# Kernel tuning notes

Hardware: AMD Instinct MI355X
Metric: run time of the kernel (lower is better)

Reference implementation:

```python
import jax, jax.numpy as jnp
from jax import lax
import numpy as np

NS, NC = 12, 4            # n_state, n_ctrl
NSC = NS + NC             # tau = [x; u]
T, B = 50, 2048
U_LO, U_HI = -1.0, 1.0
LQR_ITERS = 3             # qp_iter-style outer LQR iterations
N_LS = 5                  # max_linesearch_iter
LS_DECAY = 0.5            # linesearch_decay


def setup_inputs() -> dict:
    key = jax.random.key(0)
    k0, k1, k2, k3, k4 = jax.random.split(key, 5)
    x0 = jax.random.normal(k0, (B, NS), jnp.float32)
    # PD quadratic cost: C = 0.1 * A A^T + I  (symmetric positive definite)
    A = jax.random.normal(k1, (T, B, NSC, NSC), jnp.float32) * (1.0 / np.sqrt(NSC))
    C = 0.1 * jnp.einsum('tbik,tbjk->tbij', A, A) + jnp.eye(NSC, dtype=jnp.float32)
    c = jax.random.normal(k2, (T, B, NSC), jnp.float32)
    # Near-identity stable linear dynamics x' = F [x;u] + f
    F = 0.02 * jax.random.normal(k3, (T, B, NS, NSC), jnp.float32)
    eye_pad = jnp.concatenate([0.98 * jnp.eye(NS, dtype=jnp.float32),
                               jnp.zeros((NS, NC), jnp.float32)], axis=-1)
    F = F + eye_pad
    f = 0.01 * jax.random.normal(k4, (T, B, NS), jnp.float32)
    return {'x0': x0, 'C': C, 'c': c, 'F': F, 'f': f}


def _riccati(C, c, F, f):
    """Backward Riccati recursion. Returns feedback gains K [T,B,NC,NS], k [T,B,NC]."""
    def step(carry, inp):
        V, v = carry                      # V: [B,NS,NS], v: [B,NS]
        Ct, ct, Ft, ft = inp
        FtV = jnp.einsum('bki,bkl->bil', Ft, V)          # F^T V: [B,NSC,NS]
        Q = Ct + jnp.einsum('bil,blj->bij', FtV, Ft)     # [B,NSC,NSC]
        q = ct + jnp.einsum('bki,bk->bi', Ft,
                            jnp.einsum('bij,bj->bi', V, ft) + v)
        Qxx, Qxu = Q[:, :NS, :NS], Q[:, :NS, NS:]
        Qux, Quu = Q[:, NS:, :NS], Q[:, NS:, NS:]
        qx, qu = q[:, :NS], q[:, NS:]
        rhs = jnp.concatenate([Qux, qu[:, :, None]], axis=-1)  # [B,NC,NS+1]
        sol = jnp.linalg.solve(Quu, rhs)
        K = -sol[:, :, :NS]               # [B,NC,NS]
        kk = -sol[:, :, NS]               # [B,NC]
        QxuK = jnp.einsum('bij,bjk->bik', Qxu, K)
        V_new = Qxx + QxuK + QxuK.transpose(0, 2, 1) \
            + jnp.einsum('bji,bjl,blk->bik', K, Quu, K)
        V_new = 0.5 * (V_new + V_new.transpose(0, 2, 1))
        v_new = qx + jnp.einsum('bij,bj->bi', Qxu, kk) \
            + jnp.einsum('bji,bj->bi', K, qu + jnp.einsum('bij,bj->bi', Quu, kk))
        return (V_new, v_new), (K, kk)

    Vz = jnp.zeros((C.shape[1], NS, NS), C.dtype)
    vz = jnp.zeros((C.shape[1], NS), C.dtype)
    _, (K, kk) = lax.scan(step, (Vz, vz), (C, c, F, f), reverse=True)
    return K, kk


def _rollout(alpha, x0, u_nom, K, kk, C, c, F, f):
    """Forward pass with box-clamped controls and line-search blending."""
    def step(carry, inp):
        x, cost = carry
        Ct, ct, Ft, ft, Kt, kt, unomt = inp
        u_lqr = jnp.einsum('bij,bj->bi', Kt, x) + kt
        u = jnp.clip((1.0 - alpha) * unomt + alpha * u_lqr, U_LO, U_HI)
        tau = jnp.concatenate([x, u], axis=-1)            # [B,NSC]
        cost = cost + 0.5 * jnp.einsum('bi,bij,bj->b', tau, Ct, tau) \
            + jnp.einsum('bi,bi->b', ct, tau)
        x_next = jnp.einsum('bij,bj->bi', Ft, tau) + ft
        return (x_next, cost), tau

    init = (x0, jnp.zeros(x0.shape[0], x0.dtype))
    (_, cost), taus = lax.scan(step, init, (C, c, F, f, K, kk, u_nom))
    return cost, taus  # cost [B], taus [T,B,NSC]


def reference(x0, C, c, F, f):
    alphas = LS_DECAY ** jnp.arange(N_LS, dtype=C.dtype)  # [N_LS]
    u_nom = jnp.zeros((T, x0.shape[0], NC), x0.dtype)
    taus = None
    for _ in range(LQR_ITERS):
        K, kk = _riccati(C, c, F, f)
        costs, taus_all = jax.vmap(
            lambda a: _rollout(a, x0, u_nom, K, kk, C, c, F, f))(alphas)
        # costs: [N_LS,B]; taus_all: [N_LS,T,B,NSC]. Pick best alpha per batch elem.
        best = jnp.argmin(costs, axis=0)                  # [B]
        taus = jnp.take_along_axis(taus_all,
                                   best[None, None, :, None], axis=0)[0]
        u_nom = taus[:, :, NS:]
    return taus  # [T, B, NSC] optimized trajectory [x; u]
```

## Files before the change

kernel.cpp:

```cpp
#include <hip/hip_runtime.h>
#include <math.h>

#define T_   50
#define B_   2048
#define NS_  12
#define NC_  4
#define NSC_ 16
#define LDC  20
#define TAUS_STRIDE 808

__device__ __forceinline__ float dot4f(const float4 a, const float4 b) {
    return a.x*b.x + a.y*b.y + a.z*b.z + a.w*b.w;
}
__device__ __forceinline__ void axpy4(float4& acc, float s, const float4 v) {
    acc.x += s*v.x; acc.y += s*v.y; acc.z += s*v.z; acc.w += s*v.w;
}

__device__ __forceinline__ void wsync() {
    __builtin_amdgcn_wave_barrier();
    __builtin_amdgcn_s_waitcnt(0xC07F);
    __builtin_amdgcn_wave_barrier();
}

struct RicPref { float4 rC, rAux; };

__device__ __forceinline__ RicPref ric_load(
    const float* Cg, const float* cg, const float* Fg, const float* fg,
    int t, int b, int lane)
{
    RicPref p;
    const size_t base = (size_t)t * B_ + b;
    p.rC = ((const float4*)(Cg + base*256))[lane];
    if (lane < 48)      p.rAux = ((const float4*)(Fg + base*192))[lane];
    else if (lane < 52) p.rAux = ((const float4*)(cg + base*16))[lane-48];
    else if (lane < 55) p.rAux = ((const float4*)(fg + base*12))[lane-52];
    return p;
}

__global__ __launch_bounds__(64) void riccati_kernel(
    const float* __restrict__ Cg, const float* __restrict__ cg,
    const float* __restrict__ Fg, const float* __restrict__ fg,
    float* __restrict__ Kk)
{
    const int b    = blockIdx.x;
    const int lane = threadIdx.x;

    __shared__ __align__(16) float sV[144];
    __shared__ __align__(16) float sv[12];
    __shared__ __align__(16) float sF[12*LDC];
    __shared__ __align__(16) float sC[16*LDC];
    __shared__ __align__(16) float sc[16];
    __shared__ __align__(16) float sf[12];
    __shared__ __align__(16) float sP[12*LDC];
    __shared__ __align__(16) float sQ[16*LDC];
    __shared__ __align__(16) float sq[16];
    __shared__ __align__(16) float stmp[12];
    __shared__ __align__(16) float sK[48];
    __shared__ __align__(16) float skk[4];
    __shared__ __align__(16) float sM[144];

    for (int i = lane; i < 144; i += 64) sV[i] = 0.f;
    if (lane < 12) sv[lane] = 0.f;

    RicPref cur = ric_load(Cg, cg, Fg, fg, T_-1, b, lane);
    wsync();

    for (int t = T_ - 1; t >= 0; --t) {
        const size_t base = (size_t)t * B_ + b;

        wsync();
        {
            const int row = lane >> 2, ch = (lane & 3) << 2;
            *(float4*)(sC + row*LDC + ch) = cur.rC;
            if (lane < 48)      *(float4*)(sF + row*LDC + ch) = cur.rAux;
            else if (lane < 52) ((float4*)sc)[lane-48] = cur.rAux;
            else if (lane < 55) ((float4*)sf)[lane-52] = cur.rAux;
        }
        RicPref nxt = ric_load(Cg, cg, Fg, fg, (t > 0) ? t-1 : 0, b, lane);
        wsync();

        if (lane < 48) {
            const int k = lane >> 2, jc = (lane & 3) << 2;
            float4 acc = make_float4(0.f,0.f,0.f,0.f);
            #pragma unroll
            for (int l = 0; l < 12; ++l) {
                axpy4(acc, sV[k*12 + l], *(const float4*)(sF + l*LDC + jc));
            }
            *(float4*)(sP + k*LDC + jc) = acc;
        } else if (lane < 60) {
            const int k = lane - 48;
            float acc = sv[k];
            #pragma unroll
            for (int l = 0; l < 12; ++l) acc += sV[k*12 + l] * sf[l];
            stmp[k] = acc;
        }
        wsync();

        {
            const int i = lane >> 2, jc = (lane & 3) << 2;
            float4 acc = *(const float4*)(sC + i*LDC + jc);
            #pragma unroll
            for (int k = 0; k < 12; ++k) {
                axpy4(acc, sF[k*LDC + i], *(const float4*)(sP + k*LDC + jc));
            }
            *(float4*)(sQ + i*LDC + jc) = acc;
        }
        if (lane < 16) {
            float acc = sc[lane];
            #pragma unroll
            for (int k = 0; k < 12; ++k) acc += sF[k*LDC + lane] * stmp[k];
            sq[lane] = acc;
        }
        wsync();

        {
            const float* Qu = sQ + 12*LDC + 12;
            const float a00=Qu[0],      a01=Qu[1],      a02=Qu[2],      a03=Qu[3];
            const float a11=Qu[LDC+1],  a12=Qu[LDC+2],  a13=Qu[LDC+3];
            const float a22=Qu[2*LDC+2],a23=Qu[2*LDC+3],a33=Qu[3*LDC+3];
            const float l00 = sqrtf(a00), i00 = 1.f/l00;
            const float l10 = a01*i00, l20 = a02*i00, l30 = a03*i00;
            const float l11 = sqrtf(a11 - l10*l10), i11 = 1.f/l11;
            const float l21 = (a12 - l20*l10)*i11;
            const float l31 = (a13 - l30*l10)*i11;
            const float l22 = sqrtf(a22 - l20*l20 - l21*l21), i22 = 1.f/l22;
            const float l32 = (a23 - l30*l20 - l31*l21)*i22;
            const float l33 = sqrtf(a33 - l30*l30 - l31*l31 - l32*l32), i33 = 1.f/l33;
            if (lane < 13) {
                float r0, r1, r2, r3;
                if (lane < 12) {
                    r0 = sQ[12*LDC + lane]; r1 = sQ[13*LDC + lane];
                    r2 = sQ[14*LDC + lane]; r3 = sQ[15*LDC + lane];
                } else {
                    r0 = sq[12]; r1 = sq[13]; r2 = sq[14]; r3 = sq[15];
                }
                const float y0 = r0*i00;
                const float y1 = (r1 - l10*y0)*i11;
                const float y2 = (r2 - l20*y0 - l21*y1)*i22;
                const float y3 = (r3 - l30*y0 - l31*y1 - l32*y2)*i33;
                const float z3 = y3*i33;
                const float z2 = (y2 - l32*z3)*i22;
                const float z1 = (y1 - l21*z2 - l31*z3)*i11;
                const float z0 = (y0 - l10*z1 - l20*z2 - l30*z3)*i00;
                if (lane < 12) {
                    sK[0*12+lane] = -z0; sK[1*12+lane] = -z1;
                    sK[2*12+lane] = -z2; sK[3*12+lane] = -z3;
                } else {
                    skk[0] = -z0; skk[1] = -z1; skk[2] = -z2; skk[3] = -z3;
                }
            }
        }
        wsync();

        if (lane < 52) {
            (Kk + base*52)[lane] = (lane < 48) ? sK[lane] : skk[lane-48];
        }
        if (lane < 36) {
            const int i = lane / 3, jc = (lane % 3) << 2;
            float4 acc = make_float4(0.f,0.f,0.f,0.f);
            #pragma unroll
            for (int m = 0; m < 4; ++m) {
                axpy4(acc, sK[m*12 + i], *(const float4*)(sQ + (12+m)*LDC + jc));
            }
            *(float4*)(sM + i*12 + jc) = acc;
        } else if (lane < 48) {
            const int i = lane - 36;
            float acc = sq[i];
            #pragma unroll
            for (int m = 0; m < 4; ++m) acc += sQ[i*LDC + 12 + m] * skk[m];
            sv[i] = acc;
        }
        wsync();

        if (lane < 36) {
            const int i = lane / 3, jc = (lane % 3) << 2;
            const float4 q  = *(const float4*)(sQ + i*LDC + jc);
            const float4 m1 = *(const float4*)(sM + i*12 + jc);
            const float t0 = sM[(jc+0)*12 + i];
            const float t1 = sM[(jc+1)*12 + i];
            const float t2 = sM[(jc+2)*12 + i];
            const float t3 = sM[(jc+3)*12 + i];
            float4 r;
            r.x = q.x + 0.5f*(m1.x + t0);
            r.y = q.y + 0.5f*(m1.y + t1);
            r.z = q.z + 0.5f*(m1.z + t2);
            r.w = q.w + 0.5f*(m1.w + t3);
            *(float4*)(sV + i*12 + jc) = r;
        }
        cur = nxt;
    }
}

struct RollPref { float4 rC, rAux, rcf; };

__device__ __forceinline__ RollPref roll_load(
    const float* Cg, const float* cg, const float* Fg, const float* fg,
    const float* Kk, int t, int b, int lane)
{
    RollPref p;
    const size_t base = (size_t)t * B_ + b;
    p.rC = ((const float4*)(Cg + base*256))[lane];
    if (lane < 48)      p.rAux = ((const float4*)(Fg + base*192))[lane];
    else if (lane < 61) p.rAux = ((const float4*)(Kk + base*52))[lane-48];
    if (lane < 4)       p.rcf = ((const float4*)(cg + base*16))[lane];
    else if (lane < 7)  p.rcf = ((const float4*)(fg + base*12))[lane-4];
    return p;
}

__global__ __launch_bounds__(64) void rollout_kernel(
    const float* __restrict__ x0g, const float* __restrict__ Cg,
    const float* __restrict__ cg,  const float* __restrict__ Fg,
    const float* __restrict__ fg,  const float* __restrict__ Kk,
    float* __restrict__ outg)
{
    const int b    = blockIdx.x;
    const int lane = threadIdx.x;

    __shared__ __align__(16) float staus[5*TAUS_STRIDE];
    __shared__ __align__(16) float sunom[T_*NC_];
    __shared__ __align__(16) float sx[5*12];
    __shared__ __align__(16) float sx0[12];
    __shared__ __align__(16) float sC[16*LDC];
    __shared__ __align__(16) float sF[12*LDC];
    __shared__ __align__(16) float sKk[56];
    __shared__ __align__(16) float sc[16];
    __shared__ __align__(16) float sf[12];
    __shared__ float scost[5];
    __shared__ int   sbest;

    for (int i = lane; i < T_*NC_; i += 64) sunom[i] = 0.f;
    if (lane < 3) ((float4*)sx0)[lane] = ((const float4*)(x0g + b*12))[lane];

    RollPref cur = roll_load(Cg, cg, Fg, fg, Kk, 0, b, lane);
    wsync();

    for (int iter = 0; iter < 3; ++iter) {
        if (lane < 60) sx[lane] = sx0[lane % 12];
        float ca = 0.f;
        float cb = 0.f;
        wsync();

        for (int t = 0; t < T_; ++t) {
            wsync();
            {
                const int row = lane >> 2, ch = (lane & 3) << 2;
                *(float4*)(sC + row*LDC + ch) = cur.rC;
                if (lane < 48)      *(float4*)(sF + row*LDC + ch) = cur.rAux;
                else if (lane < 61) ((float4*)sKk)[lane-48] = cur.rAux;
                if (lane < 4)       ((float4*)sc)[lane]   = cur.rcf;
                else if (lane < 7)  ((float4*)sf)[lane-4] = cur.rcf;
            }
            RollPref nxt = roll_load(Cg, cg, Fg, fg, Kk,
                                     (t+1 < T_) ? t+1 : 0, b, lane);
            wsync();

            if (lane < 20) {
                const int a = lane >> 2, i = lane & 3;
                const float* Kr = sKk + i*12;
                const float* xa = sx  + a*12;
                float ulqr = dot4f(*(const float4*)(Kr  ), *(const float4*)(xa  ))
                           + dot4f(*(const float4*)(Kr+4), *(const float4*)(xa+4))
                           + dot4f(*(const float4*)(Kr+8), *(const float4*)(xa+8))
                           + sKk[48 + i];
                const float al = ldexpf(1.0f, -a);
                float u = (1.f - al) * sunom[t*4 + i] + al * ulqr;
                u = fminf(1.f, fmaxf(-1.f, u));
                staus[a*TAUS_STRIDE + t*16 + 12 + i] = u;
            } else if (lane >= 32 && lane < 47) {
                const int idx = lane - 32;
                const int a = idx / 3, ch = (idx % 3) << 2;
                *(float4*)(staus + a*TAUS_STRIDE + t*16 + ch) =
                    *(const float4*)(sx + a*12 + ch);
            }
            wsync();

            {
                const int a = lane >> 4, i = lane & 15;
                const float* tau = staus + a*TAUS_STRIDE + t*16;
                const float* Cr  = sC + i*LDC;
                float acc = 0.f;
                #pragma unroll
                for (int chv = 0; chv < 4; ++chv) {
                    acc += dot4f(*(const float4*)(Cr + 4*chv),
                                 *(const float4*)(tau + 4*chv));
                }
                ca += (0.5f*acc + sc[i]) * tau[i];
            }
            if (lane < 16) {
                const int i = lane;
                const float* tau = staus + 4*TAUS_STRIDE + t*16;
                const float* Cr  = sC + i*LDC;
                float acc = 0.f;
                #pragma unroll
                for (int chv = 0; chv < 4; ++chv) {
                    acc += dot4f(*(const float4*)(Cr + 4*chv),
                                 *(const float4*)(tau + 4*chv));
                }
                cb += (0.5f*acc + sc[i]) * tau[i];
            }

            if (lane < 60) {
                const int a = lane / 12, i = lane - a*12;
                const float* tau = staus + a*TAUS_STRIDE + t*16;
                const float* Fr  = sF + i*LDC;
                float acc = sf[i];
                #pragma unroll
                for (int chv = 0; chv < 4; ++chv) {
                    acc += dot4f(*(const float4*)(Fr + 4*chv),
                                 *(const float4*)(tau + 4*chv));
                }
                sx[a*12 + i] = acc;
            }
            cur = nxt;
        }

        #pragma unroll
        for (int off = 1; off < 16; off <<= 1) {
            ca += __shfl_xor(ca, off, 16);
            cb += __shfl_xor(cb, off, 16);
        }
        if ((lane & 15) == 0) scost[lane >> 4] = ca;
        if (lane == 0) scost[4] = cb;
        wsync();
        if (lane == 0) {
            int bi = 0; float bc = scost[0];
            #pragma unroll
            for (int a = 1; a < 5; ++a) {
                if (scost[a] < bc) { bc = scost[a]; bi = a; }
            }
            sbest = bi;
        }
        wsync();
        const int best = sbest;

        for (int idx = lane; idx < T_*NC_; idx += 64) {
            const int tt = idx >> 2, i = idx & 3;
            sunom[idx] = staus[best*TAUS_STRIDE + tt*16 + 12 + i];
        }
        if (iter == 2) {
            for (int idx = lane; idx < T_*NSC_; idx += 64) {
                const int tt = idx >> 4, j = idx & 15;
                outg[((size_t)tt*B_ + b)*16 + j] = staus[best*TAUS_STRIDE + tt*16 + j];
            }
        }
        wsync();
    }
}

extern "C" void kernel_launch(void* const* d_in, const int* in_sizes, int n_in,
                              void* d_out, int out_size, void* d_ws, size_t ws_size,
                              hipStream_t stream) {
    const float* x0 = (const float*)d_in[0];
    const float* C  = (const float*)d_in[1];
    const float* c  = (const float*)d_in[2];
    const float* F  = (const float*)d_in[3];
    const float* f  = (const float*)d_in[4];
    float* out = (float*)d_out;
    float* Kk  = (float*)d_ws;

    riccati_kernel<<<B_, 64, 0, stream>>>(C, c, F, f, Kk);
    rollout_kernel<<<B_, 64, 0, stream>>>(x0, C, c, F, f, Kk, out);
}
```

Baseline: 426.2 us.

## Split rollout kernel across two waves with merged cost/dynamics tasks

Each rollout block now runs two waves. One wave streams C and the other streams F, K, c and f. The per-step work is redistributed so the 80 cost dot-products and 60 next-state products are spread across 128 threads. The separate sx buffer is dropped, and next states are written straight into the tau buffer for the next timestep. This is meant to shorten the serial per-step critical path and split the load traffic, at the cost of a workgroup barrier (s_barrier) per phase instead of wave-only syncs.

```diff
diff --git a/kernel.cpp b/kernel.cpp
--- a/kernel.cpp
+++ b/kernel.cpp
@@ -20,6 +20,10 @@
     __builtin_amdgcn_wave_barrier();
     __builtin_amdgcn_s_waitcnt(0xC07F);
     __builtin_amdgcn_wave_barrier();
+}
+
+__device__ __forceinline__ void bsync() {
+    asm volatile("s_waitcnt lgkmcnt(0)\n\ts_barrier" ::: "memory");
 }
 
 struct RicPref { float4 rC, rAux; };
@@ -191,34 +195,35 @@
     }
 }
 
-struct RollPref { float4 rC, rAux, rcf; };
-
-__device__ __forceinline__ RollPref roll_load(
-    const float* Cg, const float* cg, const float* Fg, const float* fg,
-    const float* Kk, int t, int b, int lane)
+struct RollAux { float4 r1, r2; };
+
+__device__ __forceinline__ RollAux aux_load(
+    const float* cg, const float* Fg, const float* fg, const float* Kk,
+    int t, int b, int lane)
 {
-    RollPref p;
+    RollAux p;
     const size_t base = (size_t)t * B_ + b;
-    p.rC = ((const float4*)(Cg + base*256))[lane];
-    if (lane < 48)      p.rAux = ((const float4*)(Fg + base*192))[lane];
-    else if (lane < 61) p.rAux = ((const float4*)(Kk + base*52))[lane-48];
-    if (lane < 4)       p.rcf = ((const float4*)(cg + base*16))[lane];
-    else if (lane < 7)  p.rcf = ((const float4*)(fg + base*12))[lane-4];
+    if (lane < 48)      p.r1 = ((const float4*)(Fg + base*192))[lane];
+    else if (lane < 61) p.r1 = ((const float4*)(Kk + base*52))[lane-48];
+    else                p.r1 = ((const float4*)(cg + base*16))[lane-61];
+    if (lane == 0)      p.r2 = ((const float4*)(cg + base*16))[3];
+    else if (lane < 4)  p.r2 = ((const float4*)(fg + base*12))[lane-1];
     return p;
 }
 
-__global__ __launch_bounds__(64) void rollout_kernel(
+__global__ __launch_bounds__(128, 4) void rollout_kernel(
     const float* __restrict__ x0g, const float* __restrict__ Cg,
     const float* __restrict__ cg,  const float* __restrict__ Fg,
     const float* __restrict__ fg,  const float* __restrict__ Kk,
     float* __restrict__ outg)
 {
     const int b    = blockIdx.x;
-    const int lane = threadIdx.x;
+    const int tid  = threadIdx.x;
+    const int wave = tid >> 6;
+    const int lane = tid & 63;
 
     __shared__ __align__(16) float staus[5*TAUS_STRIDE];
     __shared__ __align__(16) float sunom[T_*NC_];
-    __shared__ __align__(16) float sx[5*12];
     __shared__ __align__(16) float sx0[12];
     __shared__ __align__(16) float sC[16*LDC];
     __shared__ __align__(16) float sF[12*LDC];
@@ -228,101 +233,103 @@
     __shared__ float scost[5];
     __shared__ int   sbest;
 
-    for (int i = lane; i < T_*NC_; i += 64) sunom[i] = 0.f;
-    if (lane < 3) ((float4*)sx0)[lane] = ((const float4*)(x0g + b*12))[lane];
-
-    RollPref cur = roll_load(Cg, cg, Fg, fg, Kk, 0, b, lane);
-    wsync();
+    const int  task    = wave*64 + lane;
+    const bool is_cost = task < 80;
+    int a1, i1;
+    if (is_cost) { a1 = task >> 4; i1 = task & 15; }
+    else { const int v = task - 80; a1 = v / 12; i1 = v - a1*12; }
+    const float* row1  = (is_cost ? (const float*)sC : (const float*)sF) + i1*LDC;
+    const float* add1  = (is_cost ? (const float*)sc : (const float*)sf) + i1;
+    float*       taub1 = staus + a1*TAUS_STRIDE;
+
+    const int    iT    = (lane < 12) ? lane : 0;
+    const float* rowT  = sF + iT*LDC;
+    float*       taubT = staus + 4*TAUS_STRIDE;
+
+    const int    aA  = (lane < 20) ? (lane >> 2) : 0;
+    const int    iA  = lane & 3;
+    const float  alA = ldexpf(1.0f, -aA);
+    const float* KrA = sKk + iA*12;
+    float*       tauA = staus + aA*TAUS_STRIDE;
+
+    for (int i = tid; i < T_*NC_; i += 128) sunom[i] = 0.f;
+    if (tid < 3) ((float4*)sx0)[tid] = ((const float4*)(x0g + (size_t)b*12))[tid];
+
+    float4  curC;
+    RollAux curA;
+    if (wave == 0) curC = ((const float4*)(Cg + (size_t)b*256))[lane];
+    else           curA = aux_load(cg, Fg, fg, Kk, 0, b, lane);
+    bsync();
 
     for (int iter = 0; iter < 3; ++iter) {
-        if (lane < 60) sx[lane] = sx0[lane % 12];
+        if (tid < 15) {
+            const int a = tid / 3, ch = (tid % 3) << 2;
+            *(float4*)(staus + a*TAUS_STRIDE + ch) = *(const float4*)(sx0 + ch);
+        }
         float ca = 0.f;
-        float cb = 0.f;
-        wsync();
+        int toff = 0;
 
         for (int t = 0; t < T_; ++t) {
-            wsync();
+            bsync();
+            if (wave == 0) {
+                const int row = lane >> 2, ch = (lane & 3) << 2;
+                *(float4*)(sC + row*LDC + ch) = curC;
+                curC = ((const float4*)(Cg +
+                          ((size_t)((t+1 < T_) ? t+1 : 0) * B_ + b)*256))[lane];
+            } else {
+                {
+                    const int row = lane >> 2, ch = (lane & 3) << 2;
+                    if (lane < 48)      *(float4*)(sF + row*LDC + ch) = curA.r1;
+                    else if (lane < 61) ((float4*)sKk)[lane-48] = curA.r1;
+                    else                ((float4*)sc)[lane-61]  = curA.r1;
+                    if (lane == 0)      ((float4*)sc)[3] = curA.r2;
+                    else if (lane < 4)  ((float4*)sf)[lane-1] = curA.r2;
+                }
+                curA = aux_load(cg, Fg, fg, Kk, (t+1 < T_) ? t+1 : 0, b, lane);
+                wsync();
+                if (lane < 20) {
+                    const float* x = tauA + toff;
+                    float ulqr = dot4f(*(const float4*)(KrA+0), *(const float4*)(x+0))
+                               + dot4f(*(const float4*)(KrA+4), *(const float4*)(x+4))
+                               + dot4f(*(const float4*)(KrA+8), *(const float4*)(x+8))
+                               + sKk[48 + iA];
+                    float u = (1.f - alA)*sunom[t*4 + iA] + alA*ulqr;
+                    u = fminf(1.f, fmaxf(-1.f, u));
+                    tauA[toff + 12 + iA] = u;
+                }
+            }
+            bsync();
+
+            const bool tnl = (t != T_-1);
             {
-                const int row = lane >> 2, ch = (lane & 3) << 2;
-                *(float4*)(sC + row*LDC + ch) = cur.rC;
-                if (lane < 48)      *(float4*)(sF + row*LDC + ch) = cur.rAux;
-                else if (lane < 61) ((float4*)sKk)[lane-48] = cur.rAux;
-                if (lane < 4)       ((float4*)sc)[lane]   = cur.rcf;
-                else if (lane < 7)  ((float4*)sf)[lane-4] = cur.rcf;
-            }
-            RollPref nxt = roll_load(Cg, cg, Fg, fg, Kk,
-                                     (t+1 < T_) ? t+1 : 0, b, lane);
-            wsync();
-
-            if (lane < 20) {
-                const int a = lane >> 2, i = lane & 3;
-                const float* Kr = sKk + i*12;
-                const float* xa = sx  + a*12;
-                float ulqr = dot4f(*(const float4*)(Kr  ), *(const float4*)(xa  ))
-                           + dot4f(*(const float4*)(Kr+4), *(const float4*)(xa+4))
-                           + dot4f(*(const float4*)(Kr+8), *(const float4*)(xa+8))
-                           + sKk[48 + i];
-                const float al = ldexpf(1.0f, -a);
-                float u = (1.f - al) * sunom[t*4 + i] + al * ulqr;
-                u = fminf(1.f, fmaxf(-1.f, u));
-                staus[a*TAUS_STRIDE + t*16 + 12 + i] = u;
-            } else if (lane >= 32 && lane < 47) {
-                const int idx = lane - 32;
-                const int a = idx / 3, ch = (idx % 3) << 2;
-                *(float4*)(staus + a*TAUS_STRIDE + t*16 + ch) =
-                    *(const float4*)(sx + a*12 + ch);
-            }
-            wsync();
-
-            {
-                const int a = lane >> 4, i = lane & 15;
-                const float* tau = staus + a*TAUS_STRIDE + t*16;
-                const float* Cr  = sC + i*LDC;
-                float acc = 0.f;
-                #pragma unroll
-                for (int chv = 0; chv < 4; ++chv) {
-                    acc += dot4f(*(const float4*)(Cr + 4*chv),
-                                 *(const float4*)(tau + 4*chv));
-                }
-                ca += (0.5f*acc + sc[i]) * tau[i];
-            }
-            if (lane < 16) {
-                const int i = lane;
-                const float* tau = staus + 4*TAUS_STRIDE + t*16;
-                const float* Cr  = sC + i*LDC;
-                float acc = 0.f;
-                #pragma unroll
-                for (int chv = 0; chv < 4; ++chv) {
-                    acc += dot4f(*(const float4*)(Cr + 4*chv),
-                                 *(const float4*)(tau + 4*chv));
-                }
-                cb += (0.5f*acc + sc[i]) * tau[i];
-            }
-
-            if (lane < 60) {
-                const int a = lane / 12, i = lane - a*12;
-                const float* tau = staus + a*TAUS_STRIDE + t*16;
-                const float* Fr  = sF + i*LDC;
-                float acc = sf[i];
-                #pragma unroll
-                for (int chv = 0; chv < 4; ++chv) {
-                    acc += dot4f(*(const float4*)(Fr + 4*chv),
-                                 *(const float4*)(tau + 4*chv));
-                }
-                sx[a*12 + i] = acc;
-            }
-            cur = nxt;
+                const float* tau = taub1 + toff;
+                const float  av  = add1[0];
+                float acc = is_cost ? 0.f : av;
+                acc += dot4f(*(const float4*)(row1+ 0), *(const float4*)(tau+ 0));
+                acc += dot4f(*(const float4*)(row1+ 4), *(const float4*)(tau+ 4));
+                acc += dot4f(*(const float4*)(row1+ 8), *(const float4*)(tau+ 8));
+                acc += dot4f(*(const float4*)(row1+12), *(const float4*)(tau+12));
+                if (is_cost)  ca += (0.5f*acc + av) * tau[i1];
+                else if (tnl) taub1[toff + 16 + i1] = acc;
+            }
+            if (wave == 0 && lane < 12 && tnl) {
+                const float* tau = taubT + toff;
+                float acc = sf[iT];
+                acc += dot4f(*(const float4*)(rowT+ 0), *(const float4*)(tau+ 0));
+                acc += dot4f(*(const float4*)(rowT+ 4), *(const float4*)(tau+ 4));
+                acc += dot4f(*(const float4*)(rowT+ 8), *(const float4*)(tau+ 8));
+                acc += dot4f(*(const float4*)(rowT+12), *(const float4*)(tau+12));
+                taubT[toff + 16 + iT] = acc;
+            }
+            toff += 16;
         }
 
         #pragma unroll
-        for (int off = 1; off < 16; off <<= 1) {
-            ca += __shfl_xor(ca, off, 16);
-            cb += __shfl_xor(cb, off, 16);
-        }
-        if ((lane & 15) == 0) scost[lane >> 4] = ca;
-        if (lane == 0) scost[4] = cb;
-        wsync();
-        if (lane == 0) {
+        for (int off = 1; off < 16; off <<= 1) ca += __shfl_xor(ca, off, 16);
+        if (wave == 0) { if ((lane & 15) == 0) scost[lane >> 4] = ca; }
+        else if (lane == 0) scost[4] = ca;
+        bsync();
+        if (tid == 0) {
             int bi = 0; float bc = scost[0];
             #pragma unroll
             for (int a = 1; a < 5; ++a) {
@@ -330,20 +337,20 @@
             }
             sbest = bi;
         }
-        wsync();
+        bsync();
         const int best = sbest;
 
-        for (int idx = lane; idx < T_*NC_; idx += 64) {
+        for (int idx = tid; idx < T_*NC_; idx += 128) {
             const int tt = idx >> 2, i = idx & 3;
             sunom[idx] = staus[best*TAUS_STRIDE + tt*16 + 12 + i];
         }
         if (iter == 2) {
-            for (int idx = lane; idx < T_*NSC_; idx += 64) {
+            for (int idx = tid; idx < T_*NSC_; idx += 128) {
                 const int tt = idx >> 4, j = idx & 15;
                 outg[((size_t)tt*B_ + b)*16 + j] = staus[best*TAUS_STRIDE + tt*16 + j];
             }
         }
-        wsync();
+        bsync();
     }
 }
 
@@ -359,5 +366,5 @@
     float* Kk  = (float*)d_ws;
 
     riccati_kernel<<<B_, 64, 0, stream>>>(C, c, F, f, Kk);
-    rollout_kernel<<<B_, 64, 0, stream>>>(x0, C, c, F, f, Kk, out);
-}
+    rollout_kernel<<<B_, 128, 0, stream>>>(x0, C, c, F, f, Kk, out);
+}
```

Result: slower. 444.2 us (+4.2%).
